# Performance work log

Hardware: AMD Instinct MI355X
Metric: run time of the kernel (lower is better)

The kernel has to match this reference:

```python
import jax, jax.numpy as jnp
import numpy as np

N_HEADS = 16
MAX_REL = 64  # max_relative_pos_len


def setup_inputs() -> dict:
    key = jax.random.key(0)
    ks = jax.random.split(key, 8)
    B, S, D = 2, 2048, 1024
    d = D // N_HEADS
    sc = 0.02
    return {
        "hidden_states": jax.random.normal(ks[0], (B, S, D), jnp.float32),
        "attention_mask": jnp.zeros((B, 1, 1, S), jnp.float32),
        "Wq": jax.random.normal(ks[1], (D, D), jnp.float32) * sc,
        "bq": jnp.zeros((D,), jnp.float32),
        "Wk": jax.random.normal(ks[2], (D, D), jnp.float32) * sc,
        "bk": jnp.zeros((D,), jnp.float32),
        "Wv": jax.random.normal(ks[3], (D, D), jnp.float32) * sc,
        "bv": jnp.zeros((D,), jnp.float32),
        "emb_k": jax.random.normal(ks[4], (2 * MAX_REL + 1, d), jnp.float32) * sc,
        "emb_v": jax.random.normal(ks[5], (2 * MAX_REL + 1, d), jnp.float32) * sc,
    }


def reference(hidden_states, attention_mask, Wq, bq, Wk, bk, Wv, bv, emb_k, emb_v):
    B, S, D = hidden_states.shape
    H = N_HEADS
    d = D // H
    scale = 1.0 / jnp.sqrt(jnp.asarray(d, hidden_states.dtype))

    def heads(x):  # [B,S,D] -> [B,H,S,d]
        return x.reshape(B, S, H, d).transpose(0, 2, 1, 3)

    q = heads(hidden_states @ Wq + bq)
    k = heads(hidden_states @ Wk + bk)
    v = heads(hidden_states @ Wv + bv)

    # relative position indices, clamped: [S_q, S_k]
    rel_idx = jnp.clip(jnp.arange(S)[:, None] - jnp.arange(S)[None, :], -MAX_REL, MAX_REL) + MAX_REL
    rel_k = emb_k[rel_idx]  # [S, S, d]

    # content scores + relative-key bias, both scaled by 1/sqrt(d)
    scores = (jnp.einsum('bhqd,bhkd->bhqk', q, k)
              + jnp.einsum('bhqd,qkd->bhqk', q, rel_k)) * scale
    scores = scores + attention_mask
    probs = jax.nn.softmax(scores, axis=-1)  # dropout is identity at p=0

    rel_v = emb_v[rel_idx]  # [S, S, d]
    ctx = (jnp.einsum('bhqk,bhkd->bhqd', probs, v)
           + jnp.einsum('bhqk,qkd->bhqd', probs, rel_v))
    return ctx.transpose(0, 2, 1, 3).reshape(B, S, D)
```

## Files before the change

kernel.cpp:

```cpp
#include <hip/hip_runtime.h>
#include <stdint.h>

typedef unsigned short u16;
typedef __attribute__((ext_vector_type(8))) short short8;
typedef __attribute__((ext_vector_type(4))) short s16x4;
typedef __attribute__((ext_vector_type(4))) float f32x4;
typedef __attribute__((ext_vector_type(4))) unsigned short u16x4;

#define S_LEN 2048
#define NH 16
#define DMODEL 1024
#define NR 129
#define LOG2E 1.44269504f

#define MFMA(a,b,c) __builtin_amdgcn_mfma_f32_16x16x32_bf16((a),(b),(c),0,0,0)

__device__ __forceinline__ u16 f2bf(float f){
  uint32_t u = __float_as_uint(f);
  u += 0x7fff + ((u >> 16) & 1);
  return (u16)(u >> 16);
}
__device__ __forceinline__ u16 f2bfa(float f){
  return (u16)((__float_as_uint(f) + 0x8000u) >> 16);
}
__device__ __forceinline__ float bf2f(u16 h){ return __uint_as_float(((uint32_t)h) << 16); }

__device__ __forceinline__ uint32_t cvtpk(float lo, float hi){
  uint32_t r;
  asm("v_cvt_pk_bf16_f32 %0, %1, %2" : "=v"(r) : "v"(lo), "v"(hi));
  return r;
}

__device__ __forceinline__ void gl_lds16(const u16* g, u16* l){
  __builtin_amdgcn_global_load_lds((const __attribute__((address_space(1))) void*)g,
                                   (__attribute__((address_space(3))) void*)l, 16, 0, 0);
}

__global__ __launch_bounds__(256) void k_prep(const float* __restrict__ X,
                                              const float* __restrict__ Wq, const float* __restrict__ Wk,
                                              const float* __restrict__ Wv, const float* __restrict__ Wemb,
                                              const float* __restrict__ mask,
                                              u16* __restrict__ Xb, u16* __restrict__ Wt,
                                              u16* __restrict__ Eb, float* __restrict__ maskL){
  const int bid = blockIdx.x, tid = threadIdx.x;
  if (bid < 4096){
    int i = bid * 256 + tid;
    const float4* xp = (const float4*)X;
    float4 v = xp[i];
    u16x4 o; o.x = f2bf(v.x); o.y = f2bf(v.y); o.z = f2bf(v.z); o.w = f2bf(v.w);
    *(u16x4*)(Xb + (size_t)i * 4) = o;
  } else if (bid < 4864){
    int b2 = bid - 4096;
    int z = b2 >> 8;
    const float* W = (z == 0) ? Wq : (z == 1) ? Wk : Wv;
    u16* Ot = Wt + (size_t)z * 1024 * 1024;
    __shared__ float t[64][65];
    int k0 = ((b2 >> 4) & 15) * 64, n0 = (b2 & 15) * 64;
    int c = tid & 63, r0 = (tid >> 6) * 16;
    #pragma unroll
    for (int i = 0; i < 16; ++i) t[r0 + i][c] = W[(size_t)(k0 + r0 + i) * 1024 + n0 + c];
    __syncthreads();
    #pragma unroll
    for (int i = 0; i < 16; ++i) Ot[(size_t)(n0 + r0 + i) * 1024 + k0 + c] = f2bf(t[c][r0 + i]);
  } else if (bid < 4900){
    int idx = (bid - 4864) * 256 + tid;
    if (idx < 144 * 64){
      int r = idx >> 6;
      Eb[idx] = (r < NR) ? f2bf(Wemb[idx]) : (u16)0;
    }
  } else {
    int idx = (bid - 4900) * 256 + tid;
    maskL[idx] = mask[idx] * LOG2E;
  }
}

__global__ __launch_bounds__(256) void k_qkv(const u16* __restrict__ Xb, const u16* __restrict__ Wt,
                                             const float* __restrict__ bq, const float* __restrict__ bk,
                                             const float* __restrict__ bv,
                                             u16* __restrict__ Qs, u16* __restrict__ Kb, u16* __restrict__ Vt){
  const int z = blockIdx.z;
  const u16* W = Wt + (size_t)z * 1024 * 1024;
  const float* bias = (z == 0) ? bq : (z == 1) ? bk : bv;
  const float vs = (z == 0) ? 0.125f * LOG2E : 1.0f;
  const int n0 = blockIdx.x * 128, m0 = blockIdx.y * 128;
  const int tid = threadIdx.x, w = tid >> 6, lane = tid & 63, l15 = lane & 15, quad = lane >> 4;
  const int wm = (w >> 1) * 64, wn = (w & 1) * 64;
  __shared__ __attribute__((aligned(16))) u16 As[128 * 32];
  __shared__ __attribute__((aligned(16))) u16 Bs[128 * 32];
  __shared__ __attribute__((aligned(16))) u16 Ts[64][136];
  f32x4 acc[4][4];
  #pragma unroll
  for (int i = 0; i < 4; ++i)
    #pragma unroll
    for (int j = 0; j < 4; ++j) acc[i][j] = (f32x4){0.f,0.f,0.f,0.f};

  const int rA = lane >> 2, cA = (lane & 3) * 8;
  const u16* aBase = Xb + (size_t)(m0 + w * 16 + rA) * 1024 + cA;
  const u16* bBase = W  + (size_t)(n0 + w * 16 + rA) * 1024 + cA;
  u16* aDst0 = As + (w * 16) * 32;  u16* aDst1 = As + (64 + w * 16) * 32;
  u16* bDst0 = Bs + (w * 16) * 32;  u16* bDst1 = Bs + (64 + w * 16) * 32;

  if (z == 2){
    for (int k0 = 0; k0 < 1024; k0 += 32){
      __syncthreads();
      gl_lds16(aBase + k0,             aDst0);
      gl_lds16(aBase + 64 * 1024 + k0, aDst1);
      gl_lds16(bBase + k0,             bDst0);
      gl_lds16(bBase + 64 * 1024 + k0, bDst1);
      __syncthreads();
      short8 af[4], bfr[4];
      #pragma unroll
      for (int f = 0; f < 4; ++f){
        af[f]  = *(const short8*)(As + (wm + f * 16 + l15) * 32 + quad * 8);
        bfr[f] = *(const short8*)(Bs + (wn + f * 16 + l15) * 32 + quad * 8);
      }
      #pragma unroll
      for (int i = 0; i < 4; ++i)
        #pragma unroll
        for (int j = 0; j < 4; ++j) acc[i][j] = MFMA(af[i], bfr[j], acc[i][j]);
    }
    const int hn0 = n0 >> 6;
    const int bb = m0 >> 11, sb = m0 & 2047;
    #pragma unroll
    for (int h2 = 0; h2 < 2; ++h2){
      __syncthreads();
      if ((w & 1) == h2){
        #pragma unroll
        for (int i = 0; i < 4; ++i){
          int sl0 = (w >> 1) * 64 + i * 16 + quad * 4;
          #pragma unroll
          for (int j = 0; j < 4; ++j){
            int d = j * 16 + l15;
            float bsv = bias[n0 + h2 * 64 + d];
            u16x4 vv;
            #pragma unroll
            for (int r = 0; r < 4; ++r) vv[r] = f2bf(acc[i][j][r] + bsv);
            *(u16x4*)&Ts[d][sl0] = vv;
          }
        }
      }
      __syncthreads();
      size_t gbase = ((size_t)(bb * 16 + hn0 + h2) * 64) * S_LEN + sb;
      #pragma unroll
      for (int it = 0; it < 4; ++it){
        int c2 = tid + it * 256;
        int d = c2 >> 4, ch = (c2 & 15) * 8;
        *(short8*)(Vt + gbase + (size_t)d * S_LEN + ch) = *(const short8*)&Ts[d][ch];
      }
    }
  } else {
    for (int k0 = 0; k0 < 1024; k0 += 32){
      __syncthreads();
      gl_lds16(aBase + k0,             aDst0);
      gl_lds16(aBase + 64 * 1024 + k0, aDst1);
      gl_lds16(bBase + k0,             bDst0);
      gl_lds16(bBase + 64 * 1024 + k0, bDst1);
      __syncthreads();
      short8 af[4], bfr[4];
      #pragma unroll
      for (int f = 0; f < 4; ++f){
        af[f]  = *(const short8*)(As + (wm + f * 16 + l15) * 32 + quad * 8);
        bfr[f] = *(const short8*)(Bs + (wn + f * 16 + l15) * 32 + quad * 8);
      }
      #pragma unroll
      for (int i = 0; i < 4; ++i)
        #pragma unroll
        for (int j = 0; j < 4; ++j) acc[i][j] = MFMA(bfr[j], af[i], acc[i][j]);
    }
    u16* outp = (z == 0) ? Qs : Kb;
    #pragma unroll
    for (int i = 0; i < 4; ++i){
      int srow = m0 + wm + i * 16 + l15;
      int bb = srow >> 11, s = srow & 2047;
      #pragma unroll
      for (int j = 0; j < 4; ++j){
        int coln = n0 + wn + j * 16 + quad * 4;
        f32x4 bsv4 = *(const f32x4*)&bias[coln];
        int hh = coln >> 6, jd = coln & 63;
        u16x4 ov;
        #pragma unroll
        for (int r = 0; r < 4; ++r) ov[r] = f2bf((acc[i][j][r] + bsv4[r]) * vs);
        *(u16x4*)(outp + (((size_t)(bb * 16 + hh)) * S_LEN + s) * 64 + jd) = ov;
      }
    }
  }
}

__global__ __launch_bounds__(256, 3) void k_flash(const u16* __restrict__ QS, const u16* __restrict__ KB,
                                                  const u16* __restrict__ VT, const u16* __restrict__ EMBK,
                                                  const float* __restrict__ maskL, const float* __restrict__ embv,
                                                  float* __restrict__ out){
  const int g = blockIdx.y; const int b = g >> 4; const int h = g & 15;
  const int q0 = blockIdx.x * 64;
  const int tid = threadIdx.x;
  const int w = tid >> 6; const int lane = tid & 63;
  const int l15 = lane & 15; const int quad = lane >> 4;
  const int wm = w * 16;
  const int rqb = quad * 4;
  const int qrow = q0 + wm + l15;

  __shared__ union UKE {
    struct {
      __attribute__((aligned(16))) u16 Ks[64][72];
      __attribute__((aligned(16))) u16 Vs[64][72];
    } s;
    __attribute__((aligned(16))) u16 Evs[64][136];
  } uu;
  __shared__ __attribute__((aligned(16))) u16 QEb[4][16][132];
  __shared__ __attribute__((aligned(16))) u16 Psb[64][136];

  {
    short8 z8 = (short8){0,0,0,0,0,0,0,0};
    for (int i = tid; i < 64 * 136 / 8; i += 256) ((short8*)Psb)[i] = z8;
  }

  const int srow0 = tid >> 3;
  const int srow1 = srow0 + 32;
  const int sch = (tid & 7) * 8;
  const int c0 = ((sch & 8) ? 32 : 0) + (sch >> 4) * 4;
  const u16* kSrc = KB + (size_t)g * S_LEN * 64 + sch;
  const u16* vSrc = VT + (size_t)g * 64 * S_LEN + sch;
  const float* mBase = maskL + b * S_LEN;

  short8 kr0 = *(const short8*)(kSrc + (size_t)srow0 * 64);
  short8 kr1 = *(const short8*)(kSrc + (size_t)srow1 * 64);
  short8 vr0 = *(const short8*)(vSrc + (size_t)srow0 * S_LEN);
  short8 vr1 = *(const short8*)(vSrc + (size_t)srow1 * S_LEN);
  f32x4 mcur[4];
  #pragma unroll
  for (int fn = 0; fn < 4; ++fn) mcur[fn] = *(const f32x4*)(mBase + fn * 16 + rqb);

  const u16* qptr = QS + ((size_t)g * S_LEN + q0 + wm + l15) * 64 + quad * 8;
  short8 qa0 = *(const short8*)qptr;
  short8 qa1 = *(const short8*)(qptr + 32);

  #pragma unroll
  for (int fn = 0; fn < 9; ++fn){
    const u16* ep = EMBK + (fn * 16 + l15) * 64 + quad * 8;
    short8 eb0 = *(const short8*)ep;
    short8 eb1 = *(const short8*)(ep + 32);
    f32x4 c = (f32x4){0.f,0.f,0.f,0.f};
    c = MFMA(qa0, eb0, c);
    c = MFMA(qa1, eb1, c);
    int col = fn * 16 + l15;
    if (col < NR){
      #pragma unroll
      for (int r = 0; r < 4; ++r) QEb[w][rqb + r][col] = f2bf(c[r]);
    }
  }
  __syncthreads();

  const float qeR = bf2f(QEb[w][l15][0]);
  const float qeL = bf2f(QEb[w][l15][128]);

  short8 bones;
  {
    short one = (l15 == 0) ? (short)0x3F80 : (short)0;
    #pragma unroll
    for (int j = 0; j < 8; ++j) bones[j] = one;
  }

  f32x4 o[4];
  #pragma unroll
  for (int f = 0; f < 4; ++f) o[f] = (f32x4){0.f,0.f,0.f,0.f};
  f32x4 lacc = (f32x4){0.f,0.f,0.f,0.f};
  float ll0v[4] = {0.f,0.f,0.f,0.f};
  float ll_mx = 0.f;
  float rsb_s = 0.f;

  for (int kt = 0; kt < S_LEN; kt += 64){
    __syncthreads();
    *(short8*)&uu.s.Ks[srow0][sch] = kr0;
    *(short8*)&uu.s.Ks[srow1][sch] = kr1;
    {
      s16x4 lo = __builtin_shufflevector(vr0, vr0, 0, 1, 2, 3);
      s16x4 hi = __builtin_shufflevector(vr0, vr0, 4, 5, 6, 7);
      *(s16x4*)&uu.s.Vs[srow0][c0]      = lo;
      *(s16x4*)&uu.s.Vs[srow0][c0 + 16] = hi;
    }
    {
      s16x4 lo = __builtin_shufflevector(vr1, vr1, 0, 1, 2, 3);
      s16x4 hi = __builtin_shufflevector(vr1, vr1, 4, 5, 6, 7);
      *(s16x4*)&uu.s.Vs[srow1][c0]      = lo;
      *(s16x4*)&uu.s.Vs[srow1][c0 + 16] = hi;
    }
    __syncthreads();

    const int ktn = kt + 64;
    f32x4 mnext[4];
    if (ktn < S_LEN){
      kr0 = *(const short8*)(kSrc + (size_t)(ktn + srow0) * 64);
      kr1 = *(const short8*)(kSrc + (size_t)(ktn + srow1) * 64);
      vr0 = *(const short8*)(vSrc + (size_t)srow0 * S_LEN + ktn);
      vr1 = *(const short8*)(vSrc + (size_t)srow1 * S_LEN + ktn);
      #pragma unroll
      for (int fn = 0; fn < 4; ++fn) mnext[fn] = *(const f32x4*)(mBase + ktn + fn * 16 + rqb);
    }

    const bool leftC  = (kt <= q0 - 128);
    const bool rightC = (kt >= q0 + 128);
    const float qeadd = leftC ? qeL : (rightC ? qeR : 0.f);

    f32x4 p4[4];
    __builtin_amdgcn_s_setprio(1);
    #pragma unroll
    for (int fn = 0; fn < 4; ++fn){
      short8 kb0 = *(const short8*)&uu.s.Ks[fn * 16 + l15][quad * 8];
      short8 kb1 = *(const short8*)&uu.s.Ks[fn * 16 + l15][32 + quad * 8];
      f32x4 c = mcur[fn] + qeadd;
      c = MFMA(kb0, qa0, c);
      c = MFMA(kb1, qa1, c);
      p4[fn] = c;
    }
    __builtin_amdgcn_s_setprio(0);

    if (leftC | rightC){
      #pragma unroll
      for (int fn = 0; fn < 4; ++fn)
        #pragma unroll
        for (int r = 0; r < 4; ++r) p4[fn][r] = __builtin_amdgcn_exp2f(p4[fn][r]);
    } else {
      #pragma unroll
      for (int fn = 0; fn < 4; ++fn){
        int kbase = kt + fn * 16 + rqb;
        #pragma unroll
        for (int r = 0; r < 4; ++r){
          int dq = qrow - (kbase + r) + 64;
          int ridx = min(max(dq, 0), 128);
          float p = __builtin_amdgcn_exp2f(p4[fn][r] + bf2f(QEb[w][l15][ridx]));
          ll_mx += (dq >= 128) ? p : 0.f;
          if (dq >= 1 && dq <= 127){
            Psb[wm + l15][127 - dq] = f2bfa(p);
            rsb_s += p;
          }
          p4[fn][r] = p;
        }
      }
    }

    __builtin_amdgcn_s_setprio(1);
    #pragma unroll
    for (int fp = 0; fp < 2; ++fp){
      union { uint32_t u[4]; short8 s8; } pk;
      pk.u[0] = cvtpk(p4[2 * fp][0],     p4[2 * fp][1]);
      pk.u[1] = cvtpk(p4[2 * fp][2],     p4[2 * fp][3]);
      pk.u[2] = cvtpk(p4[2 * fp + 1][0], p4[2 * fp + 1][1]);
      pk.u[3] = cvtpk(p4[2 * fp + 1][2], p4[2 * fp + 1][3]);
      short8 pa = pk.s8;
      lacc = MFMA(pa, bones, lacc);
      #pragma unroll
      for (int fd = 0; fd < 4; ++fd){
        short8 vb = *(const short8*)&uu.s.Vs[fd * 16 + l15][quad * 16 + fp * 8];
        o[fd] = MFMA(pa, vb, o[fd]);
      }
    }
    __builtin_amdgcn_s_setprio(0);

    if (kt == q0 - 128){
      #pragma unroll
      for (int r = 0; r < 4; ++r) ll0v[r] = lacc[r];
    }
    if (ktn < S_LEN){
      #pragma unroll
      for (int fn = 0; fn < 4; ++fn) mcur[fn] = mnext[fn];
    }
  }

  __syncthreads();
  {
    int d = tid & 63, t4 = tid >> 6;
    #pragma unroll
    for (int it = 0; it < 34; ++it){
      int t = t4 + it * 4;
      float v = (t <= 126) ? embv[(size_t)(127 - t) * 64 + d] : 0.f;
      uu.Evs[d][t] = f2bf(v);
    }
  }
  __syncthreads();

  f32x4 ob[4];
  #pragma unroll
  for (int f = 0; f < 4; ++f) ob[f] = (f32x4){0.f,0.f,0.f,0.f};
  #pragma unroll
  for (int kb = 0; kb < 4; ++kb){
    short8 pa = *(const short8*)&Psb[wm + l15][kb * 32 + quad * 8];
    #pragma unroll
    for (int fd = 0; fd < 4; ++fd){
      short8 vb = *(const short8*)&uu.Evs[fd * 16 + l15][kb * 32 + quad * 8];
      ob[fd] = MFMA(pa, vb, ob[fd]);
    }
  }

  #pragma unroll
  for (int st = 16; st < 64; st <<= 1){
    ll_mx += __shfl_xor(ll_mx, st, 64);
    rsb_s += __shfl_xor(rsb_s, st, 64);
  }

  float inv[4], tl[4], trr[4];
  #pragma unroll
  for (int r = 0; r < 4; ++r){
    float L   = __shfl(lacc[r], quad << 4);
    float l0  = __shfl(ll0v[r], quad << 4);
    int src   = (quad << 4) + rqb + r;
    float lmx = __shfl(ll_mx, src);
    float rv  = __shfl(rsb_s, src);
    inv[r] = 1.f / L;
    tl[r]  = (l0 + lmx) * inv[r];
    trr[r] = 1.f - tl[r] - rv * inv[r];
  }

  #pragma unroll
  for (int fd = 0; fd < 4; ++fd){
    int dim = fd * 16 + l15;
    float evL = embv[(size_t)128 * 64 + dim];
    float evR = embv[dim];
    #pragma unroll
    for (int r = 0; r < 4; ++r){
      int row = q0 + wm + rqb + r;
      float val = (o[fd][r] + ob[fd][r]) * inv[r] + tl[r] * evL + trr[r] * evR;
      out[((size_t)(b * S_LEN + row)) * DMODEL + h * 64 + dim] = val;
    }
  }
}

extern "C" void kernel_launch(void* const* d_in, const int* in_sizes, int n_in,
                              void* d_out, int out_size, void* d_ws, size_t ws_size,
                              hipStream_t stream){
  const float* X    = (const float*)d_in[0];
  const float* mask = (const float*)d_in[1];
  const float* Wq   = (const float*)d_in[2];
  const float* bq   = (const float*)d_in[3];
  const float* Wk   = (const float*)d_in[4];
  const float* bk   = (const float*)d_in[5];
  const float* Wv   = (const float*)d_in[6];
  const float* bv   = (const float*)d_in[7];
  const float* embk = (const float*)d_in[8];
  const float* embv = (const float*)d_in[9];
  float* out = (float*)d_out;
  char* ws = (char*)d_ws;

  u16* XB   = (u16*)(ws + 0);
  u16* WT   = (u16*)(ws + 8388608);
  u16* EKB  = (u16*)(ws + 14680064);
  u16* QS   = (u16*)(ws + 14698496);
  u16* KB   = (u16*)(ws + 23087104);
  u16* VT   = (u16*)(ws + 31475712);
  float* MSL = (float*)(ws + 48252928);

  k_prep   <<<4916, 256, 0, stream>>>(X, Wq, Wk, Wv, embk, mask, XB, WT, EKB, MSL);
  k_qkv    <<<dim3(8, 32, 3), 256, 0, stream>>>(XB, WT, bq, bk, bv, QS, KB, VT);
  k_flash  <<<dim3(32, 32), 256, 0, stream>>>(QS, KB, VT, EKB, MSL, embv, out);
}
```

Measured before the change: 221.2 us.

## Double-buffer K/V via direct global-to-LDS loads with XOR swizzle and pre-permuted V

The flash kernel now stages K and V tiles with global_load_lds into double-buffered, XOR-swizzled LDS arrays. This replaces the register round-trip and the two barriers per iteration with a single barrier. The QKV kernel writes V already permuted so the MFMA operand layout can be loaded directly. The band-probability scatter into Psb moves out of the hot loop: packed bf16 probabilities for the three diagonal tiles are kept in registers and written after the loop. Psb now shares LDS with Evs, which lowers shared-memory usage, but the extra registers may raise register pressure.

```diff
diff --git a/kernel.cpp b/kernel.cpp
--- a/kernel.cpp
+++ b/kernel.cpp
@@ -3,7 +3,6 @@
 
 typedef unsigned short u16;
 typedef __attribute__((ext_vector_type(8))) short short8;
-typedef __attribute__((ext_vector_type(4))) short s16x4;
 typedef __attribute__((ext_vector_type(4))) float f32x4;
 typedef __attribute__((ext_vector_type(4))) unsigned short u16x4;
 
@@ -19,9 +18,6 @@
   uint32_t u = __float_as_uint(f);
   u += 0x7fff + ((u >> 16) & 1);
   return (u16)(u >> 16);
-}
-__device__ __forceinline__ u16 f2bfa(float f){
-  return (u16)((__float_as_uint(f) + 0x8000u) >> 16);
 }
 __device__ __forceinline__ float bf2f(u16 h){ return __uint_as_float(((uint32_t)h) << 16); }
 
@@ -77,7 +73,7 @@
 __global__ __launch_bounds__(256) void k_qkv(const u16* __restrict__ Xb, const u16* __restrict__ Wt,
                                              const float* __restrict__ bq, const float* __restrict__ bk,
                                              const float* __restrict__ bv,
-                                             u16* __restrict__ Qs, u16* __restrict__ Kb, u16* __restrict__ Vt){
+                                             u16* __restrict__ Qs, u16* __restrict__ Kb, u16* __restrict__ Vp){
   const int z = blockIdx.z;
   const u16* W = Wt + (size_t)z * 1024 * 1024;
   const float* bias = (z == 0) ? bq : (z == 1) ? bk : bv;
@@ -144,8 +140,15 @@
       #pragma unroll
       for (int it = 0; it < 4; ++it){
         int c2 = tid + it * 256;
-        int d = c2 >> 4, ch = (c2 & 15) * 8;
-        *(short8*)(Vt + gbase + (size_t)d * S_LEN + ch) = *(const short8*)&Ts[d][ch];
+        int d = c2 >> 4, m = c2 & 15;
+        int blk = (m >> 3) * 64, mb = m & 7;
+        int q = mb >> 1, f = (mb & 1) * 2;
+        const u16* lo = &Ts[d][blk + f * 16 + q * 4];
+        const u16* hi = &Ts[d][blk + (f + 1) * 16 + q * 4];
+        short8 vv;
+        #pragma unroll
+        for (int u = 0; u < 4; ++u){ vv[u] = (short)lo[u]; vv[4 + u] = (short)hi[u]; }
+        *(short8*)(Vp + gbase + (size_t)d * S_LEN + blk + mb * 8) = vv;
       }
     }
   } else {
@@ -187,7 +190,7 @@
 }
 
 __global__ __launch_bounds__(256, 3) void k_flash(const u16* __restrict__ QS, const u16* __restrict__ KB,
-                                                  const u16* __restrict__ VT, const u16* __restrict__ EMBK,
+                                                  const u16* __restrict__ VP, const u16* __restrict__ EMBK,
                                                   const float* __restrict__ maskL, const float* __restrict__ embv,
                                                   float* __restrict__ out){
   const int g = blockIdx.y; const int b = g >> 4; const int h = g & 15;
@@ -201,31 +204,31 @@
 
   __shared__ union UKE {
     struct {
-      __attribute__((aligned(16))) u16 Ks[64][72];
-      __attribute__((aligned(16))) u16 Vs[64][72];
+      __attribute__((aligned(16))) u16 K[2][4096];
+      __attribute__((aligned(16))) u16 V[2][4096];
     } s;
-    __attribute__((aligned(16))) u16 Evs[64][136];
+    struct {
+      __attribute__((aligned(16))) u16 Psb[64][128];
+      __attribute__((aligned(16))) u16 Evs[64][128];
+    } t;
   } uu;
-  __shared__ __attribute__((aligned(16))) u16 QEb[4][16][132];
-  __shared__ __attribute__((aligned(16))) u16 Psb[64][136];
+  __shared__ __attribute__((aligned(16))) u16 QEb[4][16][128];
+
+  const int lrow = lane >> 3;
+  const int lsw  = ((lane & 7) ^ lrow) * 8;
+  const u16* kS = KB + ((size_t)g * S_LEN + w * 16 + lrow) * 64 + lsw;
+  const u16* vS = VP + ((size_t)(g * 64 + w * 16 + lrow)) * S_LEN + lsw;
+  const float* mBase = maskL + b * S_LEN;
 
   {
-    short8 z8 = (short8){0,0,0,0,0,0,0,0};
-    for (int i = tid; i < 64 * 136 / 8; i += 256) ((short8*)Psb)[i] = z8;
-  }
-
-  const int srow0 = tid >> 3;
-  const int srow1 = srow0 + 32;
-  const int sch = (tid & 7) * 8;
-  const int c0 = ((sch & 8) ? 32 : 0) + (sch >> 4) * 4;
-  const u16* kSrc = KB + (size_t)g * S_LEN * 64 + sch;
-  const u16* vSrc = VT + (size_t)g * 64 * S_LEN + sch;
-  const float* mBase = maskL + b * S_LEN;
-
-  short8 kr0 = *(const short8*)(kSrc + (size_t)srow0 * 64);
-  short8 kr1 = *(const short8*)(kSrc + (size_t)srow1 * 64);
-  short8 vr0 = *(const short8*)(vSrc + (size_t)srow0 * S_LEN);
-  short8 vr1 = *(const short8*)(vSrc + (size_t)srow1 * S_LEN);
+    u16* kd = uu.s.K[0] + (w * 16) * 64;
+    u16* vd = uu.s.V[0] + (w * 16) * 64;
+    gl_lds16(kS,             kd);
+    gl_lds16(kS + 8 * 64,    kd + 512);
+    gl_lds16(vS,             vd);
+    gl_lds16(vS + 8 * S_LEN, vd + 512);
+  }
+
   f32x4 mcur[4];
   #pragma unroll
   for (int fn = 0; fn < 4; ++fn) mcur[fn] = *(const f32x4*)(mBase + fn * 16 + rqb);
@@ -234,6 +237,7 @@
   short8 qa0 = *(const short8*)qptr;
   short8 qa1 = *(const short8*)(qptr + 32);
 
+  float qeLf = 0.f;
   #pragma unroll
   for (int fn = 0; fn < 9; ++fn){
     const u16* ep = EMBK + (fn * 16 + l15) * 64 + quad * 8;
@@ -242,16 +246,24 @@
     f32x4 c = (f32x4){0.f,0.f,0.f,0.f};
     c = MFMA(qa0, eb0, c);
     c = MFMA(qa1, eb1, c);
-    int col = fn * 16 + l15;
-    if (col < NR){
-      #pragma unroll
-      for (int r = 0; r < 4; ++r) QEb[w][rqb + r][col] = f2bf(c[r]);
+    if (fn < 8){
+      #pragma unroll
+      for (int r = 0; r < 4; ++r) QEb[w][rqb + r][fn * 16 + l15] = f2bf(c[r]);
+    } else {
+      int srcl = (l15 >> 2) << 4;
+      float t0 = __shfl(c[0], srcl, 64);
+      float t1 = __shfl(c[1], srcl, 64);
+      float t2 = __shfl(c[2], srcl, 64);
+      float t3 = __shfl(c[3], srcl, 64);
+      int rr = l15 & 3;
+      float qv = (rr == 0) ? t0 : (rr == 1) ? t1 : (rr == 2) ? t2 : t3;
+      qeLf = bf2f(f2bf(qv));
     }
   }
   __syncthreads();
 
   const float qeR = bf2f(QEb[w][l15][0]);
-  const float qeL = bf2f(QEb[w][l15][128]);
+  const float qeL = qeLf;
 
   short8 bones;
   {
@@ -259,6 +271,12 @@
     #pragma unroll
     for (int j = 0; j < 8; ++j) bones[j] = one;
   }
+
+  const int rsw = l15 & 7;
+  const int kO0 = ((quad     ^ rsw) * 8);
+  const int kO1 = (((quad+4) ^ rsw) * 8);
+  const int vO0 = (((quad*2)     ^ rsw) * 8);
+  const int vO1 = (((quad*2 + 1) ^ rsw) * 8);
 
   f32x4 o[4];
   #pragma unroll
@@ -267,46 +285,35 @@
   float ll0v[4] = {0.f,0.f,0.f,0.f};
   float ll_mx = 0.f;
   float rsb_s = 0.f;
-
+  uint32_t st0[8] = {0,0,0,0,0,0,0,0};
+  uint32_t st1[8] = {0,0,0,0,0,0,0,0};
+  uint32_t st2[8] = {0,0,0,0,0,0,0,0};
+
+  int cur = 0;
   for (int kt = 0; kt < S_LEN; kt += 64){
-    __syncthreads();
-    *(short8*)&uu.s.Ks[srow0][sch] = kr0;
-    *(short8*)&uu.s.Ks[srow1][sch] = kr1;
-    {
-      s16x4 lo = __builtin_shufflevector(vr0, vr0, 0, 1, 2, 3);
-      s16x4 hi = __builtin_shufflevector(vr0, vr0, 4, 5, 6, 7);
-      *(s16x4*)&uu.s.Vs[srow0][c0]      = lo;
-      *(s16x4*)&uu.s.Vs[srow0][c0 + 16] = hi;
-    }
-    {
-      s16x4 lo = __builtin_shufflevector(vr1, vr1, 0, 1, 2, 3);
-      s16x4 hi = __builtin_shufflevector(vr1, vr1, 4, 5, 6, 7);
-      *(s16x4*)&uu.s.Vs[srow1][c0]      = lo;
-      *(s16x4*)&uu.s.Vs[srow1][c0 + 16] = hi;
-    }
-    __syncthreads();
-
     const int ktn = kt + 64;
-    f32x4 mnext[4];
+
     if (ktn < S_LEN){
-      kr0 = *(const short8*)(kSrc + (size_t)(ktn + srow0) * 64);
-      kr1 = *(const short8*)(kSrc + (size_t)(ktn + srow1) * 64);
-      vr0 = *(const short8*)(vSrc + (size_t)srow0 * S_LEN + ktn);
-      vr1 = *(const short8*)(vSrc + (size_t)srow1 * S_LEN + ktn);
-      #pragma unroll
-      for (int fn = 0; fn < 4; ++fn) mnext[fn] = *(const f32x4*)(mBase + ktn + fn * 16 + rqb);
+      u16* kd = uu.s.K[cur ^ 1] + (w * 16) * 64;
+      u16* vd = uu.s.V[cur ^ 1] + (w * 16) * 64;
+      gl_lds16(kS + (size_t)ktn * 64,       kd);
+      gl_lds16(kS + (size_t)(ktn + 8) * 64, kd + 512);
+      gl_lds16(vS + ktn,                    vd);
+      gl_lds16(vS + ktn + 8 * S_LEN,        vd + 512);
     }
 
     const bool leftC  = (kt <= q0 - 128);
     const bool rightC = (kt >= q0 + 128);
     const float qeadd = leftC ? qeL : (rightC ? qeR : 0.f);
 
+    const u16* ks = uu.s.K[cur];
     f32x4 p4[4];
     __builtin_amdgcn_s_setprio(1);
     #pragma unroll
     for (int fn = 0; fn < 4; ++fn){
-      short8 kb0 = *(const short8*)&uu.s.Ks[fn * 16 + l15][quad * 8];
-      short8 kb1 = *(const short8*)&uu.s.Ks[fn * 16 + l15][32 + quad * 8];
+      const u16* krow = ks + (fn * 16 + l15) * 64;
+      short8 kb0 = *(const short8*)(krow + kO0);
+      short8 kb1 = *(const short8*)(krow + kO1);
       f32x4 c = mcur[fn] + qeadd;
       c = MFMA(kb0, qa0, c);
       c = MFMA(kb1, qa1, c);
@@ -314,6 +321,12 @@
     }
     __builtin_amdgcn_s_setprio(0);
 
+    f32x4 mnext[4];
+    if (ktn < S_LEN){
+      #pragma unroll
+      for (int fn = 0; fn < 4; ++fn) mnext[fn] = *(const f32x4*)(mBase + ktn + fn * 16 + rqb);
+    }
+
     if (leftC | rightC){
       #pragma unroll
       for (int fn = 0; fn < 4; ++fn)
@@ -326,19 +339,18 @@
         #pragma unroll
         for (int r = 0; r < 4; ++r){
           int dq = qrow - (kbase + r) + 64;
-          int ridx = min(max(dq, 0), 128);
-          float p = __builtin_amdgcn_exp2f(p4[fn][r] + bf2f(QEb[w][l15][ridx]));
+          int ridx = min(max(dq, 0), 127);
+          float qv = (dq >= 128) ? qeL : bf2f(QEb[w][l15][ridx]);
+          float p = __builtin_amdgcn_exp2f(p4[fn][r] + qv);
           ll_mx += (dq >= 128) ? p : 0.f;
-          if (dq >= 1 && dq <= 127){
-            Psb[wm + l15][127 - dq] = f2bfa(p);
-            rsb_s += p;
-          }
+          rsb_s += (dq >= 1 && dq <= 127) ? p : 0.f;
           p4[fn][r] = p;
         }
       }
     }
 
     __builtin_amdgcn_s_setprio(1);
+    const u16* vsb = uu.s.V[cur];
     #pragma unroll
     for (int fp = 0; fp < 2; ++fp){
       union { uint32_t u[4]; short8 s8; } pk;
@@ -346,11 +358,22 @@
       pk.u[1] = cvtpk(p4[2 * fp][2],     p4[2 * fp][3]);
       pk.u[2] = cvtpk(p4[2 * fp + 1][0], p4[2 * fp + 1][1]);
       pk.u[3] = cvtpk(p4[2 * fp + 1][2], p4[2 * fp + 1][3]);
+      if (kt == q0 - 64){
+        #pragma unroll
+        for (int u4 = 0; u4 < 4; ++u4) st0[fp * 4 + u4] = pk.u[u4];
+      } else if (kt == q0){
+        #pragma unroll
+        for (int u4 = 0; u4 < 4; ++u4) st1[fp * 4 + u4] = pk.u[u4];
+      } else if (kt == q0 + 64){
+        #pragma unroll
+        for (int u4 = 0; u4 < 4; ++u4) st2[fp * 4 + u4] = pk.u[u4];
+      }
       short8 pa = pk.s8;
       lacc = MFMA(pa, bones, lacc);
+      const int vO = fp ? vO1 : vO0;
       #pragma unroll
       for (int fd = 0; fd < 4; ++fd){
-        short8 vb = *(const short8*)&uu.s.Vs[fd * 16 + l15][quad * 16 + fp * 8];
+        short8 vb = *(const short8*)(vsb + (fd * 16 + l15) * 64 + vO);
         o[fd] = MFMA(pa, vb, o[fd]);
       }
     }
@@ -364,29 +387,52 @@
       #pragma unroll
       for (int fn = 0; fn < 4; ++fn) mcur[fn] = mnext[fn];
     }
-  }
-
-  __syncthreads();
+    __syncthreads();
+    cur ^= 1;
+  }
+
   {
+    short8 z8 = (short8){0,0,0,0,0,0,0,0};
+    #pragma unroll
+    for (int i = 0; i < 4; ++i) ((short8*)uu.t.Psb)[tid + i * 256] = z8;
     int d = tid & 63, t4 = tid >> 6;
     #pragma unroll
-    for (int it = 0; it < 34; ++it){
+    for (int it = 0; it < 32; ++it){
       int t = t4 + it * 4;
       float v = (t <= 126) ? embv[(size_t)(127 - t) * 64 + d] : 0.f;
-      uu.Evs[d][t] = f2bf(v);
+      uu.t.Evs[d][(((t >> 3) ^ (d & 7)) << 3) | (t & 7)] = f2bf(v);
     }
   }
   __syncthreads();
 
+  auto bandw = [&](int ktb, const uint32_t* st){
+    #pragma unroll
+    for (int fn = 0; fn < 4; ++fn)
+      #pragma unroll
+      for (int r = 0; r < 4; ++r){
+        int dq = qrow - (ktb + fn * 16 + rqb + r) + 64;
+        if (dq >= 1 && dq <= 127){
+          int t = 127 - dq;
+          uu.t.Psb[wm + l15][(((t >> 3) ^ rsw) << 3) | (t & 7)] =
+            (u16)(st[(fn >> 1) * 4 + (fn & 1) * 2 + (r >> 1)] >> ((r & 1) * 16));
+        }
+      }
+  };
+  if (q0 >= 64) bandw(q0 - 64, st0);
+  bandw(q0, st1);
+  if (q0 + 64 < S_LEN) bandw(q0 + 64, st2);
+  __syncthreads();
+
   f32x4 ob[4];
   #pragma unroll
   for (int f = 0; f < 4; ++f) ob[f] = (f32x4){0.f,0.f,0.f,0.f};
   #pragma unroll
   for (int kb = 0; kb < 4; ++kb){
-    short8 pa = *(const short8*)&Psb[wm + l15][kb * 32 + quad * 8];
+    const int go = ((kb * 4 + quad) ^ rsw) << 3;
+    short8 pa = *(const short8*)&uu.t.Psb[wm + l15][go];
     #pragma unroll
     for (int fd = 0; fd < 4; ++fd){
-      short8 vb = *(const short8*)&uu.Evs[fd * 16 + l15][kb * 32 + quad * 8];
+      short8 vb = *(const short8*)&uu.t.Evs[fd * 16 + l15][go];
       ob[fd] = MFMA(pa, vb, ob[fd]);
     }
   }
@@ -445,10 +491,10 @@
   u16* EKB  = (u16*)(ws + 14680064);
   u16* QS   = (u16*)(ws + 14698496);
   u16* KB   = (u16*)(ws + 23087104);
-  u16* VT   = (u16*)(ws + 31475712);
+  u16* VP   = (u16*)(ws + 31475712);
   float* MSL = (float*)(ws + 48252928);
 
   k_prep   <<<4916, 256, 0, stream>>>(X, Wq, Wk, Wv, embk, mask, XB, WT, EKB, MSL);
-  k_qkv    <<<dim3(8, 32, 3), 256, 0, stream>>>(XB, WT, bq, bk, bv, QS, KB, VT);
-  k_flash  <<<dim3(32, 32), 256, 0, stream>>>(QS, KB, VT, EKB, MSL, embv, out);
-}
+  k_qkv    <<<dim3(8, 32, 3), 256, 0, stream>>>(XB, WT, bq, bk, bv, QS, KB, VP);
+  k_flash  <<<dim3(32, 32), 256, 0, stream>>>(QS, KB, VP, EKB, MSL, embv, out);
+}
```

New measurement: 235.8 us. 1.07x slower.
